# Optimization experiments

Hardware: AMD Instinct MI355X
Metric: run time of the kernel (lower is better)

## Reference

```python
import jax, jax.numpy as jnp
import numpy as np

# pywt db2 decomposition filters
DEC_LO = np.array([-0.12940952255092145, 0.22414386804185735,
                   0.836516303737469, 0.48296291314469025], dtype=np.float32)
DEC_HI = np.array([-0.48296291314469025, 0.836516303737469,
                   -0.22414386804185735, -0.12940952255092145], dtype=np.float32)

# pywt WaveletPacket2D.get_level(2, order='freq') graycode order over per-axis
# band paths: ['ll','lh','hh','hl'] -> (band at level1, band at level2), 0=low,1=high
GRAY = [(0, 0), (0, 1), (1, 1), (1, 0)]


def _pdwt_last(x, filts):
    """Single-level periodization-mode DWT along last axis.
    pywt 'per' mode (even N): out[i] = sum_j f[j] * x[(2i+1-j) mod N].
    Equivalent to circular left-pad by L-2 then VALID strided conv with the
    time-reversed filter. filts: [2, L] already reversed (lo, hi).
    Returns [..., 2, N//2] (band axis inserted before halved axis)."""
    *lead, N = x.shape
    L = filts.shape[-1]
    xe = jnp.concatenate([x[..., N - (L - 2):], x], axis=-1)  # [..., N+L-2]
    y = jax.lax.conv_general_dilated(
        xe.reshape(-1, 1, N + L - 2), filts[:, None, :],
        window_strides=(2,), padding='VALID')  # [B, 2, N//2]
    return y.reshape(*lead, 2, N // 2)


def _dwt2(x, filts):
    """2D single-level periodized DWT on the last two axes.
    x: [..., H, W] -> [..., 2(row band), 2(col band), H/2, W/2].
    Row band 1 = high-pass along axis -2 (pywt 'h' node = cH = 'da')."""
    y = _pdwt_last(x.swapaxes(-1, -2), filts)      # [..., W, 2, H/2]
    y = jnp.moveaxis(y, -2, -3).swapaxes(-1, -2)   # [..., 2, H/2, W]
    z = _pdwt_last(y, filts)                       # [..., 2, H/2, 2, W/2]
    return jnp.moveaxis(z, -2, -3)                 # [..., 2, 2, H/2, W/2]


def setup_inputs() -> dict:
    key = jax.random.key(0)
    x = jax.random.uniform(key, (3, 2048, 2048), dtype=jnp.float32)  # CHW in [0,1]
    return {"x": x, "dec_lo": jnp.asarray(DEC_LO), "dec_hi": jnp.asarray(DEC_HI)}


def reference(x, dec_lo, dec_hi):
    filts = jnp.stack([dec_lo[::-1], dec_hi[::-1]])  # time-reversed lo/hi, [2, L]
    b1 = _dwt2(x, filts)    # [C, 2, 2, H/2, W/2]            (r1, c1)
    b2 = _dwt2(b1, filts)   # [C, 2, 2, 2, 2, H/4, W/4]      (r1, c1, r2, c2)
    C = x.shape[0]
    h, w = b2.shape[-2:]
    # frequency-ordered 4x4 grid, flattened row-major, channels outermost
    bands = [b2[:, r1, c1, r2, c2] for (r1, r2) in GRAY for (c1, c2) in GRAY]
    y = jnp.stack(bands, axis=1)  # [C, 16, H/4, W/4]
    return y.reshape(C * 16, h, w)
```

## Files before the change

kernel.cpp:

```cpp
#include <hip/hip_runtime.h>

#define HH 2048
#define WW 2048
#define OH 512
#define OW 512
#define TKC 32
#define TKR 16
#define SROWS 70
#define SSZ (SROWS * TKC * 4)
#define NPAIR (SROWS * TKC)
#define NBLK 512
#define TPB 3

#define BAR()     __builtin_amdgcn_s_barrier()
#define SCHED0()  __builtin_amdgcn_sched_barrier(0)
#define WAITV(n)  asm volatile("s_waitcnt vmcnt(" #n ")" ::: "memory")
#define WAITLGKM() asm volatile("s_waitcnt lgkmcnt(0)" ::: "memory")

__device__ __forceinline__ float rfl(float v) {
    return __int_as_float(__builtin_amdgcn_readfirstlane(__float_as_int(v)));
}

__global__ __launch_bounds__(512, 4)
void wpt2_kernel(const float* __restrict__ x,
                 const float* __restrict__ dec_lo,
                 const float* __restrict__ dec_hi,
                 float* __restrict__ out) {
    __shared__ float sA[SSZ];
    __shared__ float sB[SSZ];

    const int tx  = threadIdx.x;
    const int ty  = threadIdx.y;
    const int tid = ty * TKC + tx;

    const int bid = blockIdx.x;
    const int swz = (bid & 7) * (NBLK / 8) + (bid >> 3);
    const int tile0 = swz * TPB;

    float lo[4], hi[4];
#pragma unroll
    for (int j = 0; j < 4; ++j) { lo[j] = dec_lo[j]; hi[j] = dec_hi[j]; }
    float F[4][10];
#pragma unroll
    for (int g = 0; g < 4; ++g) {
        const float* f1 = (g >= 2) ? hi : lo;
        const float* f2 = (g == 1 || g == 2) ? hi : lo;
#pragma unroll
        for (int d = 0; d < 10; ++d) F[g][d] = 0.f;
#pragma unroll
        for (int j2 = 0; j2 < 4; ++j2)
#pragma unroll
            for (int j1 = 0; j1 < 4; ++j1)
                F[g][2 * j2 + j1] = fmaf(f2[j2], f1[j1], F[g][2 * j2 + j1]);
    }
#pragma unroll
    for (int g = 0; g < 4; ++g)
#pragma unroll
        for (int d = 0; d < 10; ++d) F[g][d] = rfl(F[g][d]);

    auto gload = [&](float4 st[5][3], int tileId) {
        const int ch  = tileId >> 9;
        const int rem = tileId & 511;
        const int tcc = rem >> 5;
        const int trr = rem & 31;
        const float* xc = x + (size_t)ch * HH * WW;
#pragma unroll
        for (int k = 0; k < 5; ++k) {
            const int p = k * 512 + tid;
            if (k < 4 || p < NPAIR) {
                const int r  = p >> 5;
                const int kc = p & 31;
                int grow = 64 * trr - 6 + r;  if (grow < 0) grow += HH;
                const float* rp = xc + (size_t)grow * WW;
                const int cb = 128 * tcc + 4 * kc;
                int c0 = cb - 8;  if (c0 < 0) c0 += WW;
                int c1 = cb - 4;  if (c1 < 0) c1 += WW;
                st[k][0] = *reinterpret_cast<const float4*>(rp + c0);
                st[k][1] = *reinterpret_cast<const float4*>(rp + c1);
                st[k][2] = *reinterpret_cast<const float4*>(rp + cb);
            }
        }
    };

    auto rowfilt = [&](const float4 st[5][3], float* sbuf) {
#pragma unroll
        for (int k = 0; k < 5; ++k) {
            const int p = k * 512 + tid;
            if (k < 4 || p < NPAIR) {
                const float w[12] = {st[k][0].x, st[k][0].y, st[k][0].z, st[k][0].w,
                                     st[k][1].x, st[k][1].y, st[k][1].z, st[k][1].w,
                                     st[k][2].x, st[k][2].y, st[k][2].z, st[k][2].w};
                float s0 = 0.f, s1 = 0.f, s2 = 0.f, s3 = 0.f;
#pragma unroll
                for (int dc = 0; dc < 10; ++dc) {
                    const float v = w[11 - dc];
                    s0 = fmaf(F[0][dc], v, s0);
                    s1 = fmaf(F[1][dc], v, s1);
                    s2 = fmaf(F[2][dc], v, s2);
                    s3 = fmaf(F[3][dc], v, s3);
                }
                float4 sv; sv.x = s0; sv.y = s1; sv.z = s2; sv.w = s3;
                *reinterpret_cast<float4*>(&sbuf[p * 4]) = sv;
            }
        }
    };

    auto colpass = [&](const float* sbuf, int tileId) {
        const int ch  = tileId >> 9;
        const int rem = tileId & 511;
        const int tcc = rem >> 5;
        const int trr = rem & 31;

        __builtin_amdgcn_s_setprio(1);
        float acc[4][4];
#pragma unroll
        for (int gi = 0; gi < 4; ++gi)
#pragma unroll
            for (int gj = 0; gj < 4; ++gj) acc[gi][gj] = 0.f;

#pragma unroll
        for (int u = 0; u < 10; ++u) {
            const float4 sv = *reinterpret_cast<const float4*>(
                &sbuf[((4 * ty + u) * TKC + tx) * 4]);
            const int dr = 9 - u;
#pragma unroll
            for (int gi = 0; gi < 4; ++gi) {
                const float fr = F[gi][dr];
                acc[gi][0] = fmaf(fr, sv.x, acc[gi][0]);
                acc[gi][1] = fmaf(fr, sv.y, acc[gi][1]);
                acc[gi][2] = fmaf(fr, sv.z, acc[gi][2]);
                acc[gi][3] = fmaf(fr, sv.w, acc[gi][3]);
            }
        }

        const int kr = TKR * trr + ty;
        const int kc = TKC * tcc + tx;
        const size_t plane = (size_t)OH * OW;
        float* op = out + (size_t)(ch * 16) * plane + (size_t)kr * OW + kc;
#pragma unroll
        for (int gi = 0; gi < 4; ++gi)
#pragma unroll
            for (int gj = 0; gj < 4; ++gj)
                __builtin_nontemporal_store(acc[gi][gj],
                                            op + (size_t)(gi * 4 + gj) * plane);
        __builtin_amdgcn_s_setprio(0);
    };

    float4 st[5][3];

    gload(st, tile0 + 0);
    WAITV(0);
    rowfilt(st, sA);
    WAITLGKM(); BAR(); SCHED0();

    gload(st, tile0 + 1); SCHED0();
    colpass(sA, tile0 + 0);
    WAITV(16);
    rowfilt(st, sB);
    WAITLGKM(); BAR(); SCHED0();

    gload(st, tile0 + 2); SCHED0();
    colpass(sB, tile0 + 1);
    WAITV(16);
    rowfilt(st, sA);
    WAITLGKM(); BAR(); SCHED0();

    colpass(sA, tile0 + 2);
}

extern "C" void kernel_launch(void* const* d_in, const int* in_sizes, int n_in,
                              void* d_out, int out_size, void* d_ws, size_t ws_size,
                              hipStream_t stream) {
    const float* x      = (const float*)d_in[0];
    const float* dec_lo = (const float*)d_in[1];
    const float* dec_hi = (const float*)d_in[2];
    float* out          = (float*)d_out;

    hipLaunchKernelGGL(wpt2_kernel, dim3(NBLK), dim3(TKC, TKR), 0, stream,
                       x, dec_lo, dec_hi, out);
}
```

Measured before the change: 21.51 us.

## Give each wave a private LDS slice with halo rows to drop block barriers

Each of the 8 waves in a block now loads and row-filters its own 14-row window, covering its 8 rows plus a 6-row halo, into a private LDS slice. Its column pass reads only that slice, so the block-wide barriers, the double buffering and the priority bumps are removed. In exchange the halo rows are loaded and row-filtered redundantly per wave: 112 rows instead of 70 per tile, which adds L2 traffic and VALU work. LDS use per block also drops.

```diff
diff --git a/kernel.cpp b/kernel.cpp
--- a/kernel.cpp
+++ b/kernel.cpp
@@ -6,15 +6,14 @@
 #define OW 512
 #define TKC 32
 #define TKR 16
-#define SROWS 70
-#define SSZ (SROWS * TKC * 4)
-#define NPAIR (SROWS * TKC)
 #define NBLK 512
 #define TPB 3
+#define WROWS 14
+#define WSZF (WROWS * TKC * 4)
+#define LDSF (8 * WSZF)
 
-#define BAR()     __builtin_amdgcn_s_barrier()
-#define SCHED0()  __builtin_amdgcn_sched_barrier(0)
-#define WAITV(n)  asm volatile("s_waitcnt vmcnt(" #n ")" ::: "memory")
+#define SCHED0()   __builtin_amdgcn_sched_barrier(0)
+#define WAITV(n)   asm volatile("s_waitcnt vmcnt(" #n ")" ::: "memory")
 #define WAITLGKM() asm volatile("s_waitcnt lgkmcnt(0)" ::: "memory")
 
 __device__ __forceinline__ float rfl(float v) {
@@ -26,12 +25,14 @@
                  const float* __restrict__ dec_lo,
                  const float* __restrict__ dec_hi,
                  float* __restrict__ out) {
-    __shared__ float sA[SSZ];
-    __shared__ float sB[SSZ];
+    __shared__ float sbuf[LDSF];
 
-    const int tx  = threadIdx.x;
-    const int ty  = threadIdx.y;
-    const int tid = ty * TKC + tx;
+    const int tid  = threadIdx.x;
+    const int w    = tid >> 6;
+    const int lane = tid & 63;
+    const int tx   = lane & 31;
+    const int typ  = lane >> 5;
+    float* const ws = &sbuf[w * WSZF];
 
     const int bid = blockIdx.x;
     const int swz = (bid & 7) * (NBLK / 8) + (bid >> 3);
@@ -58,60 +59,53 @@
 #pragma unroll
         for (int d = 0; d < 10; ++d) F[g][d] = rfl(F[g][d]);
 
-    auto gload = [&](float4 st[5][3], int tileId) {
+    auto gload = [&](float4 st[7][3], int tileId) {
         const int ch  = tileId >> 9;
         const int rem = tileId & 511;
         const int tcc = rem >> 5;
         const int trr = rem & 31;
         const float* xc = x + (size_t)ch * HH * WW;
+        const int cb = 128 * tcc + 4 * tx;
+        int c0 = cb - 8;  if (c0 < 0) c0 += WW;
+        int c1 = cb - 4;  if (c1 < 0) c1 += WW;
 #pragma unroll
-        for (int k = 0; k < 5; ++k) {
-            const int p = k * 512 + tid;
-            if (k < 4 || p < NPAIR) {
-                const int r  = p >> 5;
-                const int kc = p & 31;
-                int grow = 64 * trr - 6 + r;  if (grow < 0) grow += HH;
-                const float* rp = xc + (size_t)grow * WW;
-                const int cb = 128 * tcc + 4 * kc;
-                int c0 = cb - 8;  if (c0 < 0) c0 += WW;
-                int c1 = cb - 4;  if (c1 < 0) c1 += WW;
-                st[k][0] = *reinterpret_cast<const float4*>(rp + c0);
-                st[k][1] = *reinterpret_cast<const float4*>(rp + c1);
-                st[k][2] = *reinterpret_cast<const float4*>(rp + cb);
-            }
+        for (int k = 0; k < 7; ++k) {
+            int grow = 64 * trr + 8 * w - 6 + 2 * k + typ;
+            if (grow < 0) grow += HH;
+            const float* rp = xc + (size_t)grow * WW;
+            st[k][0] = *reinterpret_cast<const float4*>(rp + c0);
+            st[k][1] = *reinterpret_cast<const float4*>(rp + c1);
+            st[k][2] = *reinterpret_cast<const float4*>(rp + cb);
         }
     };
 
-    auto rowfilt = [&](const float4 st[5][3], float* sbuf) {
+    auto rowfilt = [&](const float4 st[7][3]) {
 #pragma unroll
-        for (int k = 0; k < 5; ++k) {
-            const int p = k * 512 + tid;
-            if (k < 4 || p < NPAIR) {
-                const float w[12] = {st[k][0].x, st[k][0].y, st[k][0].z, st[k][0].w,
-                                     st[k][1].x, st[k][1].y, st[k][1].z, st[k][1].w,
-                                     st[k][2].x, st[k][2].y, st[k][2].z, st[k][2].w};
-                float s0 = 0.f, s1 = 0.f, s2 = 0.f, s3 = 0.f;
+        for (int k = 0; k < 7; ++k) {
+            const float wv[12] = {st[k][0].x, st[k][0].y, st[k][0].z, st[k][0].w,
+                                  st[k][1].x, st[k][1].y, st[k][1].z, st[k][1].w,
+                                  st[k][2].x, st[k][2].y, st[k][2].z, st[k][2].w};
+            float s0 = 0.f, s1 = 0.f, s2 = 0.f, s3 = 0.f;
 #pragma unroll
-                for (int dc = 0; dc < 10; ++dc) {
-                    const float v = w[11 - dc];
-                    s0 = fmaf(F[0][dc], v, s0);
-                    s1 = fmaf(F[1][dc], v, s1);
-                    s2 = fmaf(F[2][dc], v, s2);
-                    s3 = fmaf(F[3][dc], v, s3);
-                }
-                float4 sv; sv.x = s0; sv.y = s1; sv.z = s2; sv.w = s3;
-                *reinterpret_cast<float4*>(&sbuf[p * 4]) = sv;
+            for (int dc = 0; dc < 10; ++dc) {
+                const float v = wv[11 - dc];
+                s0 = fmaf(F[0][dc], v, s0);
+                s1 = fmaf(F[1][dc], v, s1);
+                s2 = fmaf(F[2][dc], v, s2);
+                s3 = fmaf(F[3][dc], v, s3);
             }
+            float4 sv; sv.x = s0; sv.y = s1; sv.z = s2; sv.w = s3;
+            const int r = 2 * k + typ;
+            *reinterpret_cast<float4*>(&ws[(r * TKC + tx) * 4]) = sv;
         }
     };
 
-    auto colpass = [&](const float* sbuf, int tileId) {
+    auto colpass = [&](int tileId) {
         const int ch  = tileId >> 9;
         const int rem = tileId & 511;
         const int tcc = rem >> 5;
         const int trr = rem & 31;
 
-        __builtin_amdgcn_s_setprio(1);
         float acc[4][4];
 #pragma unroll
         for (int gi = 0; gi < 4; ++gi)
@@ -121,7 +115,7 @@
 #pragma unroll
         for (int u = 0; u < 10; ++u) {
             const float4 sv = *reinterpret_cast<const float4*>(
-                &sbuf[((4 * ty + u) * TKC + tx) * 4]);
+                &ws[((4 * typ + u) * TKC + tx) * 4]);
             const int dr = 9 - u;
 #pragma unroll
             for (int gi = 0; gi < 4; ++gi) {
@@ -133,7 +127,7 @@
             }
         }
 
-        const int kr = TKR * trr + ty;
+        const int kr = TKR * trr + 2 * w + typ;
         const int kc = TKC * tcc + tx;
         const size_t plane = (size_t)OH * OW;
         float* op = out + (size_t)(ch * 16) * plane + (size_t)kr * OW + kc;
@@ -143,29 +137,28 @@
             for (int gj = 0; gj < 4; ++gj)
                 __builtin_nontemporal_store(acc[gi][gj],
                                             op + (size_t)(gi * 4 + gj) * plane);
-        __builtin_amdgcn_s_setprio(0);
     };
 
-    float4 st[5][3];
+    float4 st[7][3];
 
     gload(st, tile0 + 0);
-    WAITV(0);
-    rowfilt(st, sA);
-    WAITLGKM(); BAR(); SCHED0();
+    WAITV(0); SCHED0();
+    rowfilt(st);
+    WAITLGKM(); SCHED0();
 
     gload(st, tile0 + 1); SCHED0();
-    colpass(sA, tile0 + 0);
-    WAITV(16);
-    rowfilt(st, sB);
-    WAITLGKM(); BAR(); SCHED0();
+    colpass(tile0 + 0);
+    WAITV(16); SCHED0();
+    rowfilt(st);
+    WAITLGKM(); SCHED0();
 
     gload(st, tile0 + 2); SCHED0();
-    colpass(sB, tile0 + 1);
-    WAITV(16);
-    rowfilt(st, sA);
-    WAITLGKM(); BAR(); SCHED0();
+    colpass(tile0 + 1);
+    WAITV(16); SCHED0();
+    rowfilt(st);
+    WAITLGKM(); SCHED0();
 
-    colpass(sA, tile0 + 2);
+    colpass(tile0 + 2);
 }
 
 extern "C" void kernel_launch(void* const* d_in, const int* in_sizes, int n_in,
@@ -176,6 +169,6 @@
     const float* dec_hi = (const float*)d_in[2];
     float* out          = (float*)d_out;
 
-    hipLaunchKernelGGL(wpt2_kernel, dim3(NBLK), dim3(TKC, TKR), 0, stream,
+    hipLaunchKernelGGL(wpt2_kernel, dim3(NBLK), dim3(512), 0, stream,
                        x, dec_lo, dec_hi, out);
 }
```

Result: slower. 23.25 us (+8.1%).
